# Kernel tuning notes

Measured on AMD Instinct MI355X. Metric: run time of the kernel, lower is better.

## Reference

```python
import jax, jax.numpy as jnp
import numpy as np

B, N, D, H = 2, 1024, 1024, 16
DH = D // H
SCALE = 1.0 / DH ** 0.5
STJ_Q = 1.0
NUM_ITER = 4
CAUSAL = True
EPS = 1e-6


def setup_inputs() -> dict:
    key = jax.random.key(0)
    k1, k2, k3 = jax.random.split(key, 3)
    x = jax.random.normal(k1, (B, N, D), jnp.float32)
    Wqkv = jax.random.normal(k2, (3 * D, D), jnp.float32) / np.float32(np.sqrt(D))
    Wo = jax.random.normal(k3, (D, D), jnp.float32) / np.float32(np.sqrt(D))
    return {"x": x, "Wqkv": Wqkv, "Wo": Wo}


def stieltjes_attention(Q, K, V, scale, causal, q, num_iter):
    # Q,K,V: [B,H,N,dh]. Scores s: [B,H,N,N].
    n = Q.shape[2]
    s = jnp.einsum('bhnd,bhmd->bhnm', Q, K) * scale
    if causal:
        mask = jnp.tril(jnp.ones((n, n), bool))  # [N,N], True = attend
    else:
        mask = jnp.ones((n, n), bool)
    # Solve per-row lambda s.t. sum_j (lambda - s_j)^(-q) = 1 (Stieltjes-transform
    # normalization) with Newton iterations; masked entries contribute 0.
    s_masked = jnp.where(mask, s, -1e30)
    lam = s_masked.max(-1) + 1.0  # [B,H,N], start above max score
    for _ in range(num_iter):
        d = jnp.maximum(lam[..., None] - s, EPS)  # [B,H,N,N]
        w = jnp.where(mask, d ** (-q), 0.0)
        f = w.sum(-1) - 1.0
        fp = -q * jnp.where(mask, d ** (-q - 1.0), 0.0).sum(-1)
        lam = lam - f / fp
    d = jnp.maximum(lam[..., None] - s, EPS)
    p = jnp.where(mask, d ** (-q), 0.0)
    p = p / p.sum(-1, keepdims=True)  # final exact normalization
    return jnp.einsum('bhnm,bhmd->bhnd', p, V)


def reference(x, Wqkv, Wo):
    b, n, dmodel = x.shape
    qkv = (x @ Wqkv.T).reshape(b, n, 3, H, DH).transpose(2, 0, 3, 1, 4)
    Q, K, V = qkv[0], qkv[1], qkv[2]
    o = stieltjes_attention(Q, K, V, SCALE, CAUSAL, STJ_Q, NUM_ITER)
    o = o.transpose(0, 2, 1, 3).reshape(b, n, dmodel)
    return o @ Wo.T
```

## Files before the change

### kernel.cpp

```cpp
#include <hip/hip_runtime.h>
#include <hip/hip_bf16.h>
#include <math.h>

#define HNUM 16
#define DH 64
#define NSEQ 1024
#define BATCH 2
#define DMODEL 1024
#define SCALE 0.125f
#define EPS 1e-6f
#define NUM_ITER 4
#define SPAD_T 1080

typedef float f32x4 __attribute__((ext_vector_type(4)));
typedef short bfrag __attribute__((ext_vector_type(8)));
typedef unsigned int u32x4 __attribute__((ext_vector_type(4)));

__device__ inline float bf2f_u(unsigned int u) {
    return __builtin_bit_cast(float, u << 16);
}
__device__ inline unsigned short f2bf_u(float f) {
    return __builtin_bit_cast(unsigned short, __float2bfloat16(f));
}

__device__ inline void gload16(const __hip_bfloat16* g, __hip_bfloat16* l) {
    __builtin_amdgcn_global_load_lds(
        (const __attribute__((address_space(1))) void*)g,
        (__attribute__((address_space(3))) void*)l, 16, 0, 0);
}

__global__ __launch_bounds__(256) void cast3(const float* __restrict__ s0, __hip_bfloat16* __restrict__ d0, int n0,
                                             const float* __restrict__ s1, __hip_bfloat16* __restrict__ d1, int n1,
                                             const float* __restrict__ s2, __hip_bfloat16* __restrict__ d2, int n2) {
    const int stride = gridDim.x * blockDim.x;
    const int tot = n0 + n1 + n2;
    for (int i = blockIdx.x * blockDim.x + threadIdx.x; i < tot; i += stride) {
        const float* s; __hip_bfloat16* d; int off;
        if (i < n0)            { s = s0; d = d0; off = i; }
        else if (i < n0 + n1)  { s = s1; d = d1; off = i - n0; }
        else                   { s = s2; d = d2; off = i - n0 - n1; }
        const float4 v = *reinterpret_cast<const float4*>(&s[(size_t)off * 4]);
        ushort4 o;
        o.x = f2bf_u(v.x); o.y = f2bf_u(v.y); o.z = f2bf_u(v.z); o.w = f2bf_u(v.w);
        *reinterpret_cast<ushort4*>(&d[(size_t)off * 4]) = o;
    }
}

__global__ __launch_bounds__(256) void gemm1_qkv(const __hip_bfloat16* __restrict__ A,
                                                 const __hip_bfloat16* __restrict__ B,
                                                 __hip_bfloat16* __restrict__ qkvb,
                                                 __hip_bfloat16* __restrict__ Vt,
                                                 int M, int Nc, int K) {
    __shared__ __align__(16) __hip_bfloat16 As[64 * 64];
    __shared__ __align__(16) __hip_bfloat16 Bs[128 * 64];
    const int tid  = threadIdx.x;
    const int l    = tid & 63;
    const int wave = tid >> 6;
    const int m0 = blockIdx.y * 64, n0 = blockIdx.x * 128;
    const int wr = (wave >> 1) * 32, wc = (wave & 1) * 64;
    const int lr = l & 15;
    const int lk = (l >> 4) * 8;

    f32x4 acc[2][4];
#pragma unroll
    for (int m = 0; m < 2; ++m)
#pragma unroll
        for (int n = 0; n < 4; ++n) acc[m][n] = (f32x4){0.f, 0.f, 0.f, 0.f};

    for (int k0 = 0; k0 < K; k0 += 64) {
#pragma unroll
        for (int p = 0; p < 2; ++p) {
            const int idx = tid + p * 256;
            const int r = idx >> 3, ce = (idx & 7) * 8;
            gload16(&A[(size_t)(m0 + r) * K + k0 + ce], &As[idx * 8]);
        }
#pragma unroll
        for (int p = 0; p < 4; ++p) {
            const int idx = tid + p * 256;
            const int r = idx >> 3, ce = (idx & 7) * 8;
            gload16(&B[(size_t)(n0 + r) * K + k0 + ce], &Bs[idx * 8]);
        }
        __syncthreads();

#pragma unroll
        for (int kk = 0; kk < 64; kk += 32) {
            bfrag af[2], bfr[4];
#pragma unroll
            for (int m = 0; m < 2; ++m)
                af[m] = *reinterpret_cast<const bfrag*>(&As[(wr + m * 16 + lr) * 64 + kk + lk]);
#pragma unroll
            for (int n = 0; n < 4; ++n)
                bfr[n] = *reinterpret_cast<const bfrag*>(&Bs[(wc + n * 16 + lr) * 64 + kk + lk]);
#pragma unroll
            for (int m = 0; m < 2; ++m)
#pragma unroll
                for (int n = 0; n < 4; ++n)
                    acc[m][n] = __builtin_amdgcn_mfma_f32_16x16x32_bf16(
                        af[m], bfr[n], acc[m][n], 0, 0, 0);
        }
        __syncthreads();
    }

#pragma unroll
    for (int m = 0; m < 2; ++m) {
        const int row0 = m0 + wr + m * 16 + (l >> 4) * 4;
#pragma unroll
        for (int n = 0; n < 4; ++n) {
            const int col = n0 + wc + n * 16 + lr;
            if (col < 2048) {
#pragma unroll
                for (int j = 0; j < 4; ++j)
                    qkvb[(size_t)(row0 + j) * Nc + col] = __float2bfloat16(acc[m][n][j]);
            } else {
                const int rc = col - 2048;
                const int bh = (row0 >> 10) * 16 + (rc >> 6);
                const int d  = rc & 63;
                ushort4 pk;
                pk.x = f2bf_u(acc[m][n][0]);
                pk.y = f2bf_u(acc[m][n][1]);
                pk.z = f2bf_u(acc[m][n][2]);
                pk.w = f2bf_u(acc[m][n][3]);
                *reinterpret_cast<ushort4*>(
                    &Vt[((size_t)(bh * 64 + d)) * 1024 + (row0 & 1023)]) = pk;
            }
        }
    }
}

__global__ __launch_bounds__(256) void gemm_bt64(const __hip_bfloat16* __restrict__ A,
                                                 const __hip_bfloat16* __restrict__ B,
                                                 float* __restrict__ C,
                                                 int M, int Nc, int K) {
    __shared__ __align__(16) __hip_bfloat16 As[64 * 64];
    __shared__ __align__(16) __hip_bfloat16 Bs[64 * 64];
    const int tid  = threadIdx.x;
    const int l    = tid & 63;
    const int wave = tid >> 6;
    const int m0 = blockIdx.y * 64, n0 = blockIdx.x * 64;
    const int wr = (wave >> 1) * 32, wc = (wave & 1) * 32;
    const int lr = l & 15;
    const int lk = (l >> 4) * 8;

    f32x4 acc[2][2];
#pragma unroll
    for (int m = 0; m < 2; ++m)
#pragma unroll
        for (int n = 0; n < 2; ++n) acc[m][n] = (f32x4){0.f, 0.f, 0.f, 0.f};

    for (int k0 = 0; k0 < K; k0 += 64) {
#pragma unroll
        for (int p = 0; p < 2; ++p) {
            const int idx = tid + p * 256;
            const int r = idx >> 3, ce = (idx & 7) * 8;
            gload16(&A[(size_t)(m0 + r) * K + k0 + ce], &As[idx * 8]);
        }
#pragma unroll
        for (int p = 0; p < 2; ++p) {
            const int idx = tid + p * 256;
            const int r = idx >> 3, ce = (idx & 7) * 8;
            gload16(&B[(size_t)(n0 + r) * K + k0 + ce], &Bs[idx * 8]);
        }
        __syncthreads();

#pragma unroll
        for (int kk = 0; kk < 64; kk += 32) {
            bfrag af[2], bfr[2];
#pragma unroll
            for (int m = 0; m < 2; ++m)
                af[m] = *reinterpret_cast<const bfrag*>(&As[(wr + m * 16 + lr) * 64 + kk + lk]);
#pragma unroll
            for (int n = 0; n < 2; ++n)
                bfr[n] = *reinterpret_cast<const bfrag*>(&Bs[(wc + n * 16 + lr) * 64 + kk + lk]);
#pragma unroll
            for (int m = 0; m < 2; ++m)
#pragma unroll
                for (int n = 0; n < 2; ++n)
                    acc[m][n] = __builtin_amdgcn_mfma_f32_16x16x32_bf16(
                        af[m], bfr[n], acc[m][n], 0, 0, 0);
        }
        __syncthreads();
    }

#pragma unroll
    for (int m = 0; m < 2; ++m) {
        const int row0 = m0 + wr + m * 16 + (l >> 4) * 4;
#pragma unroll
        for (int n = 0; n < 2; ++n) {
            const int col = n0 + wc + n * 16 + lr;
#pragma unroll
            for (int j = 0; j < 4; ++j)
                C[(size_t)(row0 + j) * Nc + col] = acc[m][n][j];
        }
    }
}

template <int NQA, int NQB>
__device__ inline void newton2_wb(unsigned short* __restrict__ SA,
                                  unsigned short* __restrict__ SB,
                                  int ncolsA, int ncolsB,
                                  int limitA, int limitB, int lane) {
    constexpr int NCA = NQA * 2, NCB = NQB * 2;
    float svA[NCA * 2], svB[NCB * 2];
#pragma unroll
    for (int t = 0; t < NCA; ++t) {
        const int c = lane * 2 + t * 128;
        int ca = c;
        if (t >= NCA - 2) ca = (c < ncolsA) ? c : 0;
        const unsigned int u = *reinterpret_cast<const unsigned int*>(&SA[ca]);
        float v0 = bf2f_u(u & 0xffffu), v1 = bf2f_u(u >> 16);
        if (t >= NCA - 2) {
            v0 = (c     < ncolsA) ? v0 : -1e30f;
            v1 = (c + 1 < ncolsA) ? v1 : -1e30f;
        }
        svA[2 * t] = v0; svA[2 * t + 1] = v1;
    }
#pragma unroll
    for (int t = 0; t < NCB; ++t) {
        const int c = lane * 2 + t * 128;
        int cbm = c;
        if (t >= NCB - 2) cbm = (c < ncolsB) ? c : 0;
        const unsigned int u = *reinterpret_cast<const unsigned int*>(&SB[cbm]);
        float v0 = bf2f_u(u & 0xffffu), v1 = bf2f_u(u >> 16);
        if (t >= NCB - 2) {
            v0 = (c     < ncolsB) ? v0 : -1e30f;
            v1 = (c + 1 < ncolsB) ? v1 : -1e30f;
        }
        svB[2 * t] = v0; svB[2 * t + 1] = v1;
    }

    float mA = svA[0], mB = svB[0];
#pragma unroll
    for (int e = 1; e < 2 * NCA; ++e) mA = fmaxf(mA, svA[e]);
#pragma unroll
    for (int e = 1; e < 2 * NCB; ++e) mB = fmaxf(mB, svB[e]);
#pragma unroll
    for (int off = 32; off; off >>= 1) {
        mA = fmaxf(mA, __shfl_xor(mA, off));
        mB = fmaxf(mB, __shfl_xor(mB, off));
    }
    float lamA = mA + 1.0f, lamB = mB + 1.0f;

    for (int it = 0; it < NUM_ITER; ++it) {
        float fA = 0.f, fpA = 0.f, fB = 0.f, fpB = 0.f;
#pragma unroll
        for (int e = 0; e < 2 * NCA; ++e) {
            const float iA = __builtin_amdgcn_rcpf(fmaxf(lamA - svA[e], EPS));
            fA += iA; fpA = fmaf(iA, iA, fpA);
        }
#pragma unroll
        for (int e = 0; e < 2 * NCB; ++e) {
            const float iB = __builtin_amdgcn_rcpf(fmaxf(lamB - svB[e], EPS));
            fB += iB; fpB = fmaf(iB, iB, fpB);
        }
#pragma unroll
        for (int off = 32; off; off >>= 1) {
            fA += __shfl_xor(fA, off); fpA += __shfl_xor(fpA, off);
            fB += __shfl_xor(fB, off); fpB += __shfl_xor(fpB, off);
        }
        lamA += (fA - 1.0f) * __builtin_amdgcn_rcpf(fpA);
        lamB += (fB - 1.0f) * __builtin_amdgcn_rcpf(fpB);
    }

    float swA = 0.f, swB = 0.f;
#pragma unroll
    for (int e = 0; e < 2 * NCA; ++e) {
        svA[e] = __builtin_amdgcn_rcpf(fmaxf(lamA - svA[e], EPS)); swA += svA[e];
    }
#pragma unroll
    for (int e = 0; e < 2 * NCB; ++e) {
        svB[e] = __builtin_amdgcn_rcpf(fmaxf(lamB - svB[e], EPS)); swB += svB[e];
    }
#pragma unroll
    for (int off = 32; off; off >>= 1) {
        swA += __shfl_xor(swA, off);
        swB += __shfl_xor(swB, off);
    }
    const float iswA = __builtin_amdgcn_rcpf(swA);
    const float iswB = __builtin_amdgcn_rcpf(swB);

#pragma unroll
    for (int t = 0; t < NCA; ++t) {
        const int c = lane * 2 + t * 128;
        if (t * 128 < limitA && c < limitA) {
            const unsigned int pk = (unsigned)f2bf_u(svA[2 * t] * iswA)
                                  | ((unsigned)f2bf_u(svA[2 * t + 1] * iswA) << 16);
            *reinterpret_cast<unsigned int*>(&SA[c]) = pk;
        }
    }
#pragma unroll
    for (int t = 0; t < NCB; ++t) {
        const int c = lane * 2 + t * 128;
        if (t * 128 < limitB && c < limitB) {
            const unsigned int pk = (unsigned)f2bf_u(svB[2 * t] * iswB)
                                  | ((unsigned)f2bf_u(svB[2 * t + 1] * iswB) << 16);
            *reinterpret_cast<unsigned int*>(&SB[c]) = pk;
        }
    }
}

__global__ __launch_bounds__(512) void attn_mfma(const __hip_bfloat16* __restrict__ qkvb,
                                                 const __hip_bfloat16* __restrict__ Vt,
                                                 __hip_bfloat16* __restrict__ obf) {
    const int tid  = threadIdx.x;
    const int lane = tid & 63;
    const int wave = tid >> 6;
    const int pair = blockIdx.x & 31;
    const int bh = blockIdx.x >> 5;
    const int b = bh >> 4, h = bh & 15;
    const int qtA = pair, qtB = 63 - pair;
    const int r0A = qtA * 16, r0B = qtB * 16;
    const int sbBase = r0A + 32;

    __shared__ __align__(16) unsigned short S[16][SPAD_T];

    const size_t qbase = (size_t)(b * NSEQ) * 3072;
    const int lr  = lane & 15;
    const int lk8 = (lane >> 4) * 8;
    const int rj0 = (lane >> 4) * 4;

    const __hip_bfloat16* qrowA = qkvb + qbase + (size_t)(r0A + lr) * 3072 + h * 64;
    const __hip_bfloat16* qrowB = qkvb + qbase + (size_t)(r0B + lr) * 3072 + h * 64;
    const bfrag aA0 = *reinterpret_cast<const bfrag*>(&qrowA[lk8]);
    const bfrag aA1 = *reinterpret_cast<const bfrag*>(&qrowA[32 + lk8]);
    const bfrag aB0 = *reinterpret_cast<const bfrag*>(&qrowB[lk8]);
    const bfrag aB1 = *reinterpret_cast<const bfrag*>(&qrowB[32 + lk8]);
    const __hip_bfloat16* kglob = qkvb + qbase + 1024 + h * 64;

    const int ntA = qtA + 2, ntB = qtB + 2;
    for (int t = wave; t < ntA + ntB; t += 8) {
        const bool isA = (t < ntA);
        const int jt  = isA ? t : (t - ntA);
        const int qtX = isA ? qtA : qtB;
        const int cb  = isA ? 0 : sbBase;
        if (jt <= qtX) {
            const int jrow = jt * 16 + lr;
            const bfrag b0 = *reinterpret_cast<const bfrag*>(&kglob[(size_t)jrow * 3072 + lk8]);
            const bfrag b1 = *reinterpret_cast<const bfrag*>(&kglob[(size_t)jrow * 3072 + 32 + lk8]);
            f32x4 c = (f32x4){0.f, 0.f, 0.f, 0.f};
            c = __builtin_amdgcn_mfma_f32_16x16x32_bf16(isA ? aA0 : aB0, b0, c, 0, 0, 0);
            c = __builtin_amdgcn_mfma_f32_16x16x32_bf16(isA ? aA1 : aB1, b1, c, 0, 0, 0);
#pragma unroll
            for (int j = 0; j < 4; ++j)
                S[rj0 + j][cb + jt * 16 + lr] = f2bf_u(c[j] * SCALE);
        } else {
#pragma unroll
            for (int j = 0; j < 4; ++j)
                S[rj0 + j][cb + jt * 16 + lr] = 0;
        }
    }
    __syncthreads();

    {
        const int limitA = r0A + 16, limitB = r0B + 16;
        for (int p = 0; p < 2; ++p) {
            const int row = wave * 2 + p;
            const int ncolsA = r0A + row + 1, ncolsB = r0B + row + 1;
            if (qtA < 16)
                newton2_wb<1, 4>(&S[row][0], &S[row][sbBase],
                                 ncolsA, ncolsB, limitA, limitB, lane);
            else
                newton2_wb<2, 3>(&S[row][0], &S[row][sbBase],
                                 ncolsA, ncolsB, limitA, limitB, lane);
        }
    }
    __syncthreads();

    {
        const int tile = wave >> 2, dt = wave & 3;
        const int r0t = tile ? r0B : r0A;
        const int cb  = tile ? sbBase : 0;
        const __hip_bfloat16* vtrow = Vt + ((size_t)(bh * 64 + dt * 16 + lr)) * 1024;

        f32x4 acc0 = (f32x4){0.f, 0.f, 0.f, 0.f};
        f32x4 acc1 = (f32x4){0.f, 0.f, 0.f, 0.f};
        for (int j0 = 0; j0 <= r0t; j0 += 64) {
            {
                const bfrag pa = *reinterpret_cast<const bfrag*>(&S[lr][cb + j0 + lk8]);
                const bfrag pb = *reinterpret_cast<const bfrag*>(&vtrow[j0 + lk8]);
                acc0 = __builtin_amdgcn_mfma_f32_16x16x32_bf16(pa, pb, acc0, 0, 0, 0);
            }
            if (j0 + 32 <= r0t) {
                const bfrag pa = *reinterpret_cast<const bfrag*>(&S[lr][cb + j0 + 32 + lk8]);
                const bfrag pb = *reinterpret_cast<const bfrag*>(&vtrow[j0 + 32 + lk8]);
                acc1 = __builtin_amdgcn_mfma_f32_16x16x32_bf16(pa, pb, acc1, 0, 0, 0);
            }
        }

#pragma unroll
        for (int j = 0; j < 4; ++j) {
            const int row = rj0 + j;
            obf[(size_t)(b * NSEQ + r0t + row) * 1024 + h * 64 + dt * 16 + lr] =
                __float2bfloat16(acc0[j] + acc1[j]);
        }
    }
}

extern "C" void kernel_launch(void* const* d_in, const int* in_sizes, int n_in,
                              void* d_out, int out_size, void* d_ws, size_t ws_size,
                              hipStream_t stream) {
    const float* x    = (const float*)d_in[0];
    const float* Wqkv = (const float*)d_in[1];
    const float* Wo   = (const float*)d_in[2];
    float* out = (float*)d_out;

    const int M = BATCH * NSEQ;
    char* ws = (char*)d_ws;
    __hip_bfloat16* xbf  = (__hip_bfloat16*)ws; ws += (size_t)M * DMODEL * 2;
    __hip_bfloat16* wqbf = (__hip_bfloat16*)ws; ws += (size_t)3 * DMODEL * DMODEL * 2;
    __hip_bfloat16* wobf = (__hip_bfloat16*)ws; ws += (size_t)DMODEL * DMODEL * 2;
    __hip_bfloat16* qkvb = (__hip_bfloat16*)ws; ws += (size_t)M * 3 * DMODEL * 2;
    __hip_bfloat16* Vt   = (__hip_bfloat16*)ws; ws += (size_t)BATCH * HNUM * DH * NSEQ * 2;
    __hip_bfloat16* obf  = (__hip_bfloat16*)ws; ws += (size_t)M * DMODEL * 2;

    dim3 blk(256);
    cast3<<<2048, blk, 0, stream>>>(x, xbf, M * DMODEL / 4,
                                    Wqkv, wqbf, 3 * DMODEL * DMODEL / 4,
                                    Wo, wobf, DMODEL * DMODEL / 4);

    dim3 g1(3 * DMODEL / 128, M / 64);
    gemm1_qkv<<<g1, blk, 0, stream>>>(xbf, wqbf, qkvb, Vt, M, 3 * DMODEL, DMODEL);

    attn_mfma<<<1024, dim3(512), 0, stream>>>(qkvb, Vt, obf);

    dim3 g2(DMODEL / 64, M / 64);
    gemm_bt64<<<g2, blk, 0, stream>>>(obf, wobf, out, M, DMODEL, DMODEL);
}
```

Baseline: 108.7 us.

## Specialize Newton row lengths, prefetch K tiles, and swizzle block order

The Newton solver is now instantiated per exact count of 128-column chunks in each row, picked by a switch, instead of two coarse quarter-based variants. This avoids processing masked-out chunks at the cost of 16 template instantiations and more code size. The score loop now prefetches the next K tile's fragments before issuing the current MFMAs, and it zeroes only the single padding tile rather than looping over dead tiles. Block IDs are also remapped so that consecutive blocks land on different (batch, head) pairs, which aims to spread the uneven causal work across XCDs and CUs.

```diff
diff --git a/kernel.cpp b/kernel.cpp
--- a/kernel.cpp
+++ b/kernel.cpp
@@ -194,21 +194,20 @@
     }
 }
 
-template <int NQA, int NQB>
+template <int NCA, int NCB>
 __device__ inline void newton2_wb(unsigned short* __restrict__ SA,
                                   unsigned short* __restrict__ SB,
                                   int ncolsA, int ncolsB,
                                   int limitA, int limitB, int lane) {
-    constexpr int NCA = NQA * 2, NCB = NQB * 2;
     float svA[NCA * 2], svB[NCB * 2];
 #pragma unroll
     for (int t = 0; t < NCA; ++t) {
         const int c = lane * 2 + t * 128;
         int ca = c;
-        if (t >= NCA - 2) ca = (c < ncolsA) ? c : 0;
+        if (t == NCA - 1) ca = (c < ncolsA) ? c : 0;
         const unsigned int u = *reinterpret_cast<const unsigned int*>(&SA[ca]);
         float v0 = bf2f_u(u & 0xffffu), v1 = bf2f_u(u >> 16);
-        if (t >= NCA - 2) {
+        if (t == NCA - 1) {
             v0 = (c     < ncolsA) ? v0 : -1e30f;
             v1 = (c + 1 < ncolsA) ? v1 : -1e30f;
         }
@@ -218,10 +217,10 @@
     for (int t = 0; t < NCB; ++t) {
         const int c = lane * 2 + t * 128;
         int cbm = c;
-        if (t >= NCB - 2) cbm = (c < ncolsB) ? c : 0;
+        if (t == NCB - 1) cbm = (c < ncolsB) ? c : 0;
         const unsigned int u = *reinterpret_cast<const unsigned int*>(&SB[cbm]);
         float v0 = bf2f_u(u & 0xffffu), v1 = bf2f_u(u >> 16);
-        if (t >= NCB - 2) {
+        if (t == NCB - 1) {
             v0 = (c     < ncolsB) ? v0 : -1e30f;
             v1 = (c + 1 < ncolsB) ? v1 : -1e30f;
         }
@@ -304,8 +303,9 @@
     const int tid  = threadIdx.x;
     const int lane = tid & 63;
     const int wave = tid >> 6;
-    const int pair = blockIdx.x & 31;
-    const int bh = blockIdx.x >> 5;
+    const int bid  = ((blockIdx.x & 7) << 7) | (blockIdx.x >> 3);
+    const int pair = bid & 31;
+    const int bh   = bid >> 5;
     const int b = bh >> 4, h = bh & 15;
     const int qtA = pair, qtB = 63 - pair;
     const int r0A = qtA * 16, r0B = qtB * 16;
@@ -326,26 +326,47 @@
     const bfrag aB1 = *reinterpret_cast<const bfrag*>(&qrowB[32 + lk8]);
     const __hip_bfloat16* kglob = qkvb + qbase + 1024 + h * 64;
 
-    const int ntA = qtA + 2, ntB = qtB + 2;
-    for (int t = wave; t < ntA + ntB; t += 8) {
-        const bool isA = (t < ntA);
-        const int jt  = isA ? t : (t - ntA);
-        const int qtX = isA ? qtA : qtB;
-        const int cb  = isA ? 0 : sbBase;
-        if (jt <= qtX) {
-            const int jrow = jt * 16 + lr;
-            const bfrag b0 = *reinterpret_cast<const bfrag*>(&kglob[(size_t)jrow * 3072 + lk8]);
-            const bfrag b1 = *reinterpret_cast<const bfrag*>(&kglob[(size_t)jrow * 3072 + 32 + lk8]);
+    if (wave < 2) {
+        const int cb  = wave ? sbBase : 0;
+        const int qtX = wave ? qtB : qtA;
+        const int cs  = cb + (qtX + 1) * 16 + lr;
+#pragma unroll
+        for (int j = 0; j < 4; ++j)
+            S[rj0 + j][cs] = 0;
+    }
+
+    {
+        const int ntA1 = qtA + 1;
+        const int ntot = ntA1 + qtB + 1;
+        int t = wave;
+        bool isA = true; int jt = 0;
+        bfrag b0{}, b1{};
+        if (t < ntot) {
+            isA = (t < ntA1);
+            jt  = isA ? t : t - ntA1;
+            const __hip_bfloat16* kp = &kglob[(size_t)(jt * 16 + lr) * 3072];
+            b0 = *reinterpret_cast<const bfrag*>(&kp[lk8]);
+            b1 = *reinterpret_cast<const bfrag*>(&kp[32 + lk8]);
+        }
+        while (t < ntot) {
+            const int t2 = t + 8;
+            bool isA2 = false; int jt2 = 0;
+            bfrag nb0{}, nb1{};
+            if (t2 < ntot) {
+                isA2 = (t2 < ntA1);
+                jt2  = isA2 ? t2 : t2 - ntA1;
+                const __hip_bfloat16* kp2 = &kglob[(size_t)(jt2 * 16 + lr) * 3072];
+                nb0 = *reinterpret_cast<const bfrag*>(&kp2[lk8]);
+                nb1 = *reinterpret_cast<const bfrag*>(&kp2[32 + lk8]);
+            }
             f32x4 c = (f32x4){0.f, 0.f, 0.f, 0.f};
             c = __builtin_amdgcn_mfma_f32_16x16x32_bf16(isA ? aA0 : aB0, b0, c, 0, 0, 0);
             c = __builtin_amdgcn_mfma_f32_16x16x32_bf16(isA ? aA1 : aB1, b1, c, 0, 0, 0);
+            const int cb = isA ? 0 : sbBase;
 #pragma unroll
             for (int j = 0; j < 4; ++j)
                 S[rj0 + j][cb + jt * 16 + lr] = f2bf_u(c[j] * SCALE);
-        } else {
-#pragma unroll
-            for (int j = 0; j < 4; ++j)
-                S[rj0 + j][cb + jt * 16 + lr] = 0;
+            t = t2; isA = isA2; jt = jt2; b0 = nb0; b1 = nb1;
         }
     }
     __syncthreads();
@@ -355,12 +376,26 @@
         for (int p = 0; p < 2; ++p) {
             const int row = wave * 2 + p;
             const int ncolsA = r0A + row + 1, ncolsB = r0B + row + 1;
-            if (qtA < 16)
-                newton2_wb<1, 4>(&S[row][0], &S[row][sbBase],
-                                 ncolsA, ncolsB, limitA, limitB, lane);
-            else
-                newton2_wb<2, 3>(&S[row][0], &S[row][sbBase],
-                                 ncolsA, ncolsB, limitA, limitB, lane);
+            const int nca = (ncolsA + 127) >> 7;
+            const int ncb = (ncolsB + 127) >> 7;
+            switch ((nca - 1) * 4 + (ncb - 5)) {
+                case 0:  newton2_wb<1, 5>(&S[row][0], &S[row][sbBase], ncolsA, ncolsB, limitA, limitB, lane); break;
+                case 1:  newton2_wb<1, 6>(&S[row][0], &S[row][sbBase], ncolsA, ncolsB, limitA, limitB, lane); break;
+                case 2:  newton2_wb<1, 7>(&S[row][0], &S[row][sbBase], ncolsA, ncolsB, limitA, limitB, lane); break;
+                case 3:  newton2_wb<1, 8>(&S[row][0], &S[row][sbBase], ncolsA, ncolsB, limitA, limitB, lane); break;
+                case 4:  newton2_wb<2, 5>(&S[row][0], &S[row][sbBase], ncolsA, ncolsB, limitA, limitB, lane); break;
+                case 5:  newton2_wb<2, 6>(&S[row][0], &S[row][sbBase], ncolsA, ncolsB, limitA, limitB, lane); break;
+                case 6:  newton2_wb<2, 7>(&S[row][0], &S[row][sbBase], ncolsA, ncolsB, limitA, limitB, lane); break;
+                case 7:  newton2_wb<2, 8>(&S[row][0], &S[row][sbBase], ncolsA, ncolsB, limitA, limitB, lane); break;
+                case 8:  newton2_wb<3, 5>(&S[row][0], &S[row][sbBase], ncolsA, ncolsB, limitA, limitB, lane); break;
+                case 9:  newton2_wb<3, 6>(&S[row][0], &S[row][sbBase], ncolsA, ncolsB, limitA, limitB, lane); break;
+                case 10: newton2_wb<3, 7>(&S[row][0], &S[row][sbBase], ncolsA, ncolsB, limitA, limitB, lane); break;
+                case 11: newton2_wb<3, 8>(&S[row][0], &S[row][sbBase], ncolsA, ncolsB, limitA, limitB, lane); break;
+                case 12: newton2_wb<4, 5>(&S[row][0], &S[row][sbBase], ncolsA, ncolsB, limitA, limitB, lane); break;
+                case 13: newton2_wb<4, 6>(&S[row][0], &S[row][sbBase], ncolsA, ncolsB, limitA, limitB, lane); break;
+                case 14: newton2_wb<4, 7>(&S[row][0], &S[row][sbBase], ncolsA, ncolsB, limitA, limitB, lane); break;
+                default: newton2_wb<4, 8>(&S[row][0], &S[row][sbBase], ncolsA, ncolsB, limitA, limitB, lane); break;
+            }
         }
     }
     __syncthreads();
```

Result: no change. 107.7 us (-0.9%).
